# Performance work log

Measured on AMD Instinct MI355X. Metric: run time of the kernel, lower is better.

Reference implementation:

```python
import jax, jax.numpy as jnp
import numpy as np

N, IN, HID, OUT, HD = 512, 256, 256, 256, 64  # n_agents, in_dim, hid_dim, out_dim, head_dim (out_dim // n_heads)


def _mlp2(x, w1, b1, w2, b2):
    return jax.nn.relu(x @ w1.T + b1) @ w2.T + b2


def setup_inputs():
    key = jax.random.key(0)
    ks = jax.random.split(key, 32)
    p = lambda i, shape: jax.random.normal(ks[i], shape, dtype=jnp.float32) * 0.05
    V = jax.random.normal(ks[0], (N, IN), dtype=jnp.float32)
    adj = jax.random.randint(ks[1], (N, N), 0, 2, dtype=jnp.int32)
    adj = adj.at[jnp.arange(N), jnp.arange(N)].set(1)  # self-loops so no softmax row is all -inf
    prev_hidden = jax.random.normal(ks[2], (N, HID), dtype=jnp.float32)
    return {
        "V": V, "adj": adj, "prev_hidden": prev_hidden,
        "W1": p(3, (HID, IN)), "sa0": p(4, (HID,)), "sa1": p(5, (HID,)),
        "ce_w1": p(6, (HID, 2 * IN)), "ce_b1": p(7, (HID,)), "ce_w2": p(8, (HD, HID)), "ce_b2": p(9, (HD,)),
        "ca0": p(10, (HD,)), "ca1": p(11, (HD,)),
        "te_w1": p(12, (HID, IN + HID)), "te_b1": p(13, (HID,)), "te_w2": p(14, (HD, HID)), "te_b2": p(15, (HD,)),
        "ta0": p(16, (HD,)), "ta1": p(17, (HD,)),
        "pe_w1": p(18, (HID, 3 * IN)), "pe_b1": p(19, (HID,)), "pe_w2": p(20, (HD, HID)), "pe_b2": p(21, (HD,)),
        "pa0": p(22, (HD,)), "pa1": p(23, (HD,)),
        "W2": p(24, (OUT, HID + 2 * HD + 1)), "op_w": p(25, (OUT, OUT)), "op_b": p(26, (OUT,)),
        "ln_g": jnp.ones((OUT,), jnp.float32), "ln_b": jnp.zeros((OUT,), jnp.float32),
    }


def _forward(V, adj, prev_hidden, W1, sa0, sa1, ce_w1, ce_b1, ce_w2, ce_b2, ca0, ca1,
             te_w1, te_b1, te_w2, te_b2, ta0, ta1, pe_w1, pe_b1, pe_w2, pe_b2, pa0, pa1,
             W2, op_w, op_b, ln_g, ln_b):
    neg = -jnp.inf
    # --- branch 1: standard GAT attention ---
    Wh1 = V @ W1.T                                             # (N, HID)
    s1 = (Wh1 @ sa0)[:, None] + (Wh1 @ sa1)[None, :]           # (N, N)
    s1 = jnp.where(adj == 0, neg, s1)
    H1 = jax.nn.softmax(s1, axis=1) @ Wh1                      # (N, HID)
    # --- branch 2: causal, all ordered pairs i != j ---
    wA, wB = ce_w1[:, :IN], ce_w1[:, IN:]
    h = jax.nn.relu((V @ wA.T)[:, None, :] + (V @ wB.T)[None, :, :] + ce_b1)  # (N, N, HID)
    f = h @ ce_w2.T + ce_b2                                    # (N, N, HD)
    s2 = jnp.where(jnp.eye(N, dtype=bool), neg, f @ (ca0 + ca1))
    a2 = jax.nn.softmax(s2.reshape(-1)).reshape(N, N)          # softmax over all off-diagonal pairs
    H2 = jnp.broadcast_to(jnp.einsum('ij,ijd->d', a2, f), (N, HD))
    # --- branch 3: temporal; (N,1) scores broadcast against (N,N) causal mask ---
    tf = _mlp2(jnp.concatenate([V, prev_hidden], -1), te_w1, te_b1, te_w2, te_b2)  # (N, HD)
    ts = tf @ (ta0 + ta1)                                      # (N,)
    cmask = jnp.triu(jnp.ones((N, N), dtype=bool), 1)
    s3 = jnp.where(cmask, neg, jnp.broadcast_to(ts[:, None], (N, N)))
    H3 = jax.nn.softmax(s3, axis=1) @ tf                       # (N, HD) == prefix means of tf
    # --- branch 4: cooperative; first two neighbors in index order (zeros if < 2) ---
    pos = jnp.where(adj == 1, jnp.arange(N)[None, :], N)
    srt = jnp.sort(pos, axis=1)
    i0, i1 = srt[:, 0], srt[:, 1]
    valid = (i1 < N)[:, None]
    n0 = jnp.where(valid, V[jnp.clip(i0, 0, N - 1)], 0.0)
    n1 = jnp.where(valid, V[jnp.clip(i1, 0, N - 1)], 0.0)
    cf = _mlp2(jnp.concatenate([V, n0, n1], -1), pe_w1, pe_b1, pe_w2, pe_b2)  # (N, HD)
    # torch: softmax over dim of size 1 -> all ones, alpha^T @ cf == column sums -> (HD,)
    # then unsqueezed to (HD,1) and zero-padded to (N,1) since HD < N  (faithful to source bug)
    H4v = cf.sum(axis=0)
    H4 = jnp.concatenate([H4v, jnp.zeros((N - HD,), V.dtype)])[:, None]       # (N, 1)
    # --- combine ---
    Hc = jnp.concatenate([H1, H2, H3, H4], axis=-1) @ W2.T     # (N, OUT)
    out = Hc @ op_w.T + op_b
    mu = out.mean(-1, keepdims=True)
    var = ((out - mu) ** 2).mean(-1, keepdims=True)
    y = (out - mu) / jnp.sqrt(var + 1e-5) * ln_g + ln_b        # LayerNorm, eps=1e-5
    return jax.nn.elu(y)                                       # dropout is identity in eval


def reference(V, adj, prev_hidden, W1, sa0, sa1, ce_w1, ce_b1, ce_w2, ce_b2, ca0, ca1,
              te_w1, te_b1, te_w2, te_b2, ta0, ta1, pe_w1, pe_b1, pe_w2, pe_b2, pa0, pa1,
              W2, op_w, op_b, ln_g, ln_b):
    return _forward(V, adj, prev_hidden, W1, sa0, sa1, ce_w1, ce_b1, ce_w2, ce_b2, ca0, ca1,
                    te_w1, te_b1, te_w2, te_b2, ta0, ta1, pe_w1, pe_b1, pe_w2, pe_b2, pa0, pa1,
                    W2, op_w, op_b, ln_g, ln_b)
```

## Files before the change

kernel.cpp:

```cpp
#include <hip/hip_runtime.h>

typedef unsigned short u16;

constexpr int kN   = 512;
constexpr int kIN  = 256;
constexpr int kHID = 256;
constexpr int kHD  = 64;
constexpr int kOUT = 256;

__device__ __forceinline__ float us2f(u16 u){
  union { unsigned int i; float f; } c; c.i = ((unsigned int)u) << 16; return c.f;
}
__device__ __forceinline__ u16 f2us(float f){
  union { float f; unsigned int i; } c; c.f = f;
  unsigned int r = c.i + 0x7fff + ((c.i >> 16) & 1);
  return (u16)(r >> 16);
}

__device__ bool probe_is_f32(const unsigned int* __restrict__ V){
  __shared__ int cnt;
  if (threadIdx.x == 0) cnt = 0;
  __syncthreads();
  int c = 0;
  for (int k = threadIdx.x; k < 4096; k += 256){
    float x = us2f((u16)(V[k] & 0xffffu));
    if (!(fabsf(x) <= 32.0f)) c++;
  }
  atomicAdd(&cnt, c);
  __syncthreads();
  return cnt > 64;
}

struct ConvArgs { const void* src[23]; float* dst[23]; int n[23]; };

__global__ __launch_bounds__(256) void k_conv(ConvArgs a, const unsigned int* __restrict__ Vraw,
                                              const int* __restrict__ adj, int* __restrict__ flag,
                                              float* __restrict__ Xp, float* __restrict__ e1v)
{
  int b = blockIdx.x, tid = threadIdx.x;
  bool f32 = probe_is_f32(Vraw);
  if (b < 256){
    if (b == 0){
      if (tid == 0) *flag = f32 ? 1 : 0;
      e1v[tid] = 0.f; e1v[tid + 256] = 0.f;
    }
    int t = b*256 + tid;
    const int stride = 65536;
    for (int s = 0; s < 23; ++s){
      int n4 = a.n[s] >> 2;
      float4* d = (float4*)a.dst[s];
      if (f32){
        const float4* sf = (const float4*)a.src[s];
        for (int i = t; i < n4; i += stride) d[i] = sf[i];
      } else {
        const ushort4* sb = (const ushort4*)a.src[s];
        for (int i = t; i < n4; i += stride){
          ushort4 u = sb[i];
          d[i] = make_float4(us2f(u.x), us2f(u.y), us2f(u.z), us2f(u.w));
        }
      }
    }
  } else {
    __shared__ unsigned long long msk[8];
    __shared__ int sj[2];
    int i = b - 256;
    int w = tid >> 6, lane = tid & 63;
    unsigned long long m0 = __ballot(adj[(size_t)i*kN + tid] != 0);
    unsigned long long m1 = __ballot(adj[(size_t)i*kN + 256 + tid] != 0);
    if (lane == 0){ msk[w] = m0; msk[4 + w] = m1; }
    __syncthreads();
    if (tid == 0){
      int j0 = -1, j1 = -1;
      for (int c = 0; c < 8 && j1 < 0; ++c){
        unsigned long long m = msk[c];
        while (m && j1 < 0){
          int bb = __builtin_ctzll(m);
          int j = c*64 + bb;
          if (j0 < 0) j0 = j; else j1 = j;
          m &= m - 1;
        }
      }
      if (j1 < 0) j0 = -1;
      sj[0] = j0; sj[1] = j1;
    }
    __syncthreads();
    int j0 = sj[0], j1 = sj[1];
    const float* Vf = (const float*)Vraw;
    const u16*  Vb = (const u16*)Vraw;
    auto rdV = [&](int r, int k)->float{
      return f32 ? Vf[(size_t)r*kIN + k] : us2f(Vb[(size_t)r*kIN + k]);
    };
    Xp[(size_t)i*768 + tid]       = rdV(i, tid);
    Xp[(size_t)i*768 + 256 + tid] = (j0 >= 0) ? rdV(j0, tid) : 0.f;
    Xp[(size_t)i*768 + 512 + tid] = (j1 >= 0) ? rdV(j1, tid) : 0.f;
  }
}

__device__ __forceinline__ float blk_red(float v, float* tmp, bool isMax){
  int lane = threadIdx.x & 63, wv = threadIdx.x >> 6;
  #pragma unroll
  for (int o = 32; o > 0; o >>= 1){
    float t = __shfl_down(v, o, 64);
    v = isMax ? fmaxf(v, t) : (v + t);
  }
  __syncthreads();
  if (lane == 0) tmp[wv] = v;
  __syncthreads();
  float r = tmp[0];
  for (int i = 1; i < 4; ++i) r = isMax ? fmaxf(r, tmp[i]) : (r + tmp[i]);
  return r;
}

struct WSP {
  const int* adj; const int* flag; void* out;
  float *Vf,*prevf,*W1f,*sa1f,*cw1f,*cb1f,*cw2f,*cb2f,*ca0f,*ca1f;
  float *tw1f,*tb1f,*tw2f,*tb2f,*pw1f,*pb1f,*pw2f,*pb2f;
  float *W2f,*opwf,*opbf,*lngf,*lnbf;
  float *tw2t,*pw2t,*W2c,*W2midt,*w384v,*c2v;
  float *Wh1,*e1v,*minv,*invzv,*wadj,*Hc,*Am,*Bm,*uvec,*beta;
  float *s2,*maxp,*zp,*MZ,*gsum;
  float *htp0,*htp1,*hpp0,*hpp1,*hpp2,*hidden_t,*hidden_p;
  float *tfm,*cfm,*H4v,*Xp,*out2,*out3;
};

struct GSeg2 { const float* X; const float* W; float* C; int ldx, ldw, ldc, K; };
struct GArgs2 { GSeg2 s[8]; const float* sa1; float* e1; };

__global__ __launch_bounds__(256) void k_gemmA(GArgs2 ga)
{
  __shared__ __align__(16) float Xs[2][32][68];
  __shared__ __align__(16) float Ws[2][32][68];
  const GSeg2 sg = ga.s[blockIdx.y];
  const int tm = blockIdx.x & 7;
  const int tn = blockIdx.x >> 3;
  const int i0 = tm << 6;
  const int n0 = tn << 6;
  const int tid = threadIdx.x;

  const int xrow = tid >> 3;
  const int xk   = (tid & 7) << 2;
  const int rg = (tid >> 4) << 2;
  const int cg = (tid & 15) << 2;

  const float* Xb = sg.X + (size_t)i0 * sg.ldx;
  const float* Wb = sg.W + (size_t)n0 * sg.ldw;

  float4 xr0, xr1, wr0, wr1;
  auto loadT = [&](int kt){
    xr0 = *(const float4*)(Xb + (size_t)xrow * sg.ldx + kt + xk);
    xr1 = *(const float4*)(Xb + (size_t)(xrow+32) * sg.ldx + kt + xk);
    wr0 = *(const float4*)(Wb + (size_t)xrow * sg.ldw + kt + xk);
    wr1 = *(const float4*)(Wb + (size_t)(xrow+32) * sg.ldw + kt + xk);
  };
  auto writeT = [&](int bu){
    Xs[bu][xk+0][xrow] = xr0.x;  Xs[bu][xk+1][xrow] = xr0.y;
    Xs[bu][xk+2][xrow] = xr0.z;  Xs[bu][xk+3][xrow] = xr0.w;
    Xs[bu][xk+0][xrow+32] = xr1.x;  Xs[bu][xk+1][xrow+32] = xr1.y;
    Xs[bu][xk+2][xrow+32] = xr1.z;  Xs[bu][xk+3][xrow+32] = xr1.w;
    Ws[bu][xk+0][xrow]    = wr0.x; Ws[bu][xk+1][xrow]    = wr0.y;
    Ws[bu][xk+2][xrow]    = wr0.z; Ws[bu][xk+3][xrow]    = wr0.w;
    Ws[bu][xk+0][xrow+32] = wr1.x; Ws[bu][xk+1][xrow+32] = wr1.y;
    Ws[bu][xk+2][xrow+32] = wr1.z; Ws[bu][xk+3][xrow+32] = wr1.w;
  };

  loadT(0); writeT(0); __syncthreads();

  float acc[4][4] = {};
  const int nkt = sg.K >> 5;
  for (int t = 0; t < nkt; ++t){
    if (t + 1 < nkt) loadT((t + 1) << 5);
    const int bu = t & 1;
    #pragma unroll
    for (int kk = 0; kk < 32; ++kk){
      const float4 av = *(const float4*)&Xs[bu][kk][rg];
      const float4 bv = *(const float4*)&Ws[bu][kk][cg];
      acc[0][0]+=av.x*bv.x; acc[0][1]+=av.x*bv.y; acc[0][2]+=av.x*bv.z; acc[0][3]+=av.x*bv.w;
      acc[1][0]+=av.y*bv.x; acc[1][1]+=av.y*bv.y; acc[1][2]+=av.y*bv.z; acc[1][3]+=av.y*bv.w;
      acc[2][0]+=av.z*bv.x; acc[2][1]+=av.z*bv.y; acc[2][2]+=av.z*bv.z; acc[2][3]+=av.z*bv.w;
      acc[3][0]+=av.w*bv.x; acc[3][1]+=av.w*bv.y; acc[3][2]+=av.w*bv.z; acc[3][3]+=av.w*bv.w;
    }
    if (t + 1 < nkt) writeT((t + 1) & 1);
    __syncthreads();
  }

  #pragma unroll
  for (int ri = 0; ri < 4; ++ri)
    *(float4*)(sg.C + (size_t)(i0 + rg + ri) * sg.ldc + (n0 + cg)) =
      make_float4(acc[ri][0], acc[ri][1], acc[ri][2], acc[ri][3]);

  if (blockIdx.y == 0){
    int cb = n0 + cg;
    float s0 = ga.sa1[cb], s1 = ga.sa1[cb+1], s2v = ga.sa1[cb+2], s3 = ga.sa1[cb+3];
    #pragma unroll
    for (int ri = 0; ri < 4; ++ri){
      float v = acc[ri][0]*s0 + acc[ri][1]*s1 + acc[ri][2]*s2v + acc[ri][3]*s3;
      v += __shfl_xor(v, 1, 16);
      v += __shfl_xor(v, 2, 16);
      v += __shfl_xor(v, 4, 16);
      v += __shfl_xor(v, 8, 16);
      if ((tid & 15) == 0) atomicAdd(&ga.e1[i0 + rg + ri], v);
    }
  }
}

struct GS32 { const float* X; const float* W; float* C; int ldx, ldw, ldc, K;
              const float* c2; const float* w384; const float* h4; int bkn; };

__device__ __forceinline__ void gemm32_body(const GS32 sg, int tm, int tn, int tid,
                                            float* Xs, float* Ws)
{
  const int i0 = tm << 5, n0 = tn << 5;
  const int xrow = tid >> 3;
  const int xk = (tid & 7) << 2;
  const int rg = (tid >> 4) << 1;
  const int cg = (tid & 15) << 1;
  const float* Xb = sg.X + (size_t)i0 * sg.ldx;
  const float* Wb = sg.bkn ? (sg.W + n0) : (sg.W + (size_t)n0 * sg.ldw);
  float h4r = 0.f;
  if (sg.h4){ int i = i0 + xrow; h4r = (i < 64) ? sg.h4[i] : 0.f; }
  float4 xr, wr;
  auto loadT = [&](int kt){
    xr = *(const float4*)(Xb + (size_t)xrow * sg.ldx + kt + xk);
    if (sg.bkn) wr = *(const float4*)(Wb + (size_t)(kt + xrow) * sg.ldw + xk);
    else        wr = *(const float4*)(Wb + (size_t)xrow * sg.ldw + kt + xk);
    if (sg.c2){
      float4 c = *(const float4*)(sg.c2 + kt + xk);
      float4 w3 = *(const float4*)(sg.w384 + kt + xk);
      xr.x += c.x + h4r*w3.x; xr.y += c.y + h4r*w3.y;
      xr.z += c.z + h4r*w3.z; xr.w += c.w + h4r*w3.w;
    }
  };
  auto writeT = [&](int bu){
    float* xs = Xs + bu*1152;
    xs[(xk+0)*36 + xrow] = xr.x; xs[(xk+1)*36 + xrow] = xr.y;
    xs[(xk+2)*36 + xrow] = xr.z; xs[(xk+3)*36 + xrow] = xr.w;
    float* wsp = Ws + bu*1152;
    if (sg.bkn){
      wsp[xrow*36 + xk+0] = wr.x; wsp[xrow*36 + xk+1] = wr.y;
      wsp[xrow*36 + xk+2] = wr.z; wsp[xrow*36 + xk+3] = wr.w;
    } else {
      wsp[(xk+0)*36 + xrow] = wr.x; wsp[(xk+1)*36 + xrow] = wr.y;
      wsp[(xk+2)*36 + xrow] = wr.z; wsp[(xk+3)*36 + xrow] = wr.w;
    }
  };
  loadT(0); writeT(0); __syncthreads();
  float a00=0,a01=0,a10=0,a11=0;
  const int nkt = sg.K >> 5;
  for (int t = 0; t < nkt; ++t){
    if (t+1 < nkt) loadT((t+1) << 5);
    const float* xs = Xs + (t&1)*1152;
    const float* wsp = Ws + (t&1)*1152;
    #pragma unroll
    for (int kk = 0; kk < 32; ++kk){
      float2 av = *(const float2*)&xs[kk*36 + rg];
      float2 bv = *(const float2*)&wsp[kk*36 + cg];
      a00 += av.x*bv.x; a01 += av.x*bv.y;
      a10 += av.y*bv.x; a11 += av.y*bv.y;
    }
    if (t+1 < nkt) writeT((t+1)&1);
    __syncthreads();
  }
  float* cp = sg.C + (size_t)(i0+rg)*sg.ldc + n0 + cg;
  *(float2*)cp = make_float2(a00, a01);
  *(float2*)(cp + sg.ldc) = make_float2(a10, a11);
}

__global__ __launch_bounds__(256) void k_stage2(WSP w)
{
  __shared__ float st[64*65];
  int b = blockIdx.x, tid = threadIdx.x;
  if (b < 128){
    int f = b*256 + tid;
    int c4 = f & 63;
    {
      float4 a = ((const float4*)w.htp0)[f], bb = ((const float4*)w.htp1)[f];
      float4 bi = ((const float4*)w.tb1f)[c4];
      ((float4*)w.hidden_t)[f] = make_float4(
        fmaxf(a.x+bb.x+bi.x,0.f), fmaxf(a.y+bb.y+bi.y,0.f),
        fmaxf(a.z+bb.z+bi.z,0.f), fmaxf(a.w+bb.w+bi.w,0.f));
    }
    {
      float4 a = ((const float4*)w.hpp0)[f], bb = ((const float4*)w.hpp1)[f];
      float4 c = ((const float4*)w.hpp2)[f];
      float4 bi = ((const float4*)w.pb1f)[c4];
      ((float4*)w.hidden_p)[f] = make_float4(
        fmaxf(a.x+bb.x+c.x+bi.x,0.f), fmaxf(a.y+bb.y+c.y+bi.y,0.f),
        fmaxf(a.z+bb.z+c.z+bi.z,0.f), fmaxf(a.w+bb.w+c.w+bi.w,0.f));
    }
  } else if (b < 640){
    float* red = st;
    int i = b - 128;
    int m0 = w.adj[(size_t)i*kN + tid];
    int m1 = w.adj[(size_t)i*kN + tid + 256];
    float ea = w.e1v[tid], eb = w.e1v[tid+256];
    float v0 = m0 ? ea : -1e30f;
    float v1 = m1 ? eb : -1e30f;
    float m = blk_red(fmaxf(v0, v1), red, true);
    float z = blk_red((m0 ? expf(ea-m) : 0.f) + (m1 ? expf(eb-m) : 0.f), red, false);
    if (tid == 0){ w.minv[i] = m; w.invzv[i] = 1.0f / z; }
  } else if (b == 640){
    if (tid < 64){ st[tid] = w.ca0f[tid] + w.ca1f[tid]; w.H4v[tid] = 0.f; }
    __syncthreads();
    float a = 0.f;
    for (int d = 0; d < kHD; ++d) a += w.cw2f[(size_t)d*kHID + tid] * st[d];
    w.uvec[tid] = a;
    if (tid == 0){
      float bsum = 0.f;
      for (int d = 0; d < kHD; ++d) bsum += w.cb2f[d] * st[d];
      *w.beta = bsum;
    }
  } else if (b < 643){
    const float* src = (b == 641) ? w.tw2f : w.pw2f;
    float* dst = (b == 641) ? w.tw2t : w.pw2t;
    for (int ch = 0; ch < 4; ++ch){
      __syncthreads();
      #pragma unroll
      for (int e = 0; e < 16; ++e){
        int lin = e*256 + tid;
        int r = lin >> 6, c = lin & 63;
        st[r*65 + c] = src[(size_t)r*256 + ch*64 + c];
      }
      __syncthreads();
      #pragma unroll
      for (int e = 0; e < 16; ++e){
        int lin = e*256 + tid;
        int kc = lin >> 6, dd = lin & 63;
        dst[(size_t)(ch*64 + kc)*64 + dd] = st[dd*65 + kc];
      }
    }
  } else if (b < 707){
    int o0 = (b - 643) * 4;
    for (int r = 0; r < 4; ++r){
      int o = o0 + r;
      const float* src = w.W2f + (size_t)o * 385;
      float* dst = w.W2c + (size_t)o * 320;
      for (int c = tid; c < 320; c += 256)
        dst[c] = src[(c < 256) ? c : c + 64];
    }
  } else if (b < 723){
    int d0 = (b - 707) * 4;
    #pragma unroll
    for (int dd = 0; dd < 4; ++dd)
      w.W2midt[(size_t)(d0+dd)*256 + tid] = w.W2f[(size_t)tid*385 + 256 + d0 + dd];
  } else {
    w.w384v[tid] = w.W2f[(size_t)tid*385 + 384];
  }
}

__global__ __launch_bounds__(256) void k_stage3(WSP w)
{
  __shared__ __align__(16) float smem3[4*256 + 256];
  int b = blockIdx.x, tid = threadIdx.x;
  if (b < 64){
    int m = b >> 5, grp = b & 31;
    const float* X  = m ? w.hidden_p : w.hidden_t;
    const float* Wt = m ? w.pw2t : w.tw2t;
    const float* bi = m ? w.pb2f : w.tb2f;
    float* C = m ? w.cfm : w.tfm;
    int i0 = grp*16 + (tid >> 6)*4;
    int d = tid & 63;
    const float* x0 = X + (size_t)i0*256;
    const float* x1 = x0 + 256;
    const float* x2 = x0 + 512;
    const float* x3 = x0 + 768;
    float a0=0.f, a1=0.f, a2=0.f, a3=0.f;
    for (int k = 0; k < 256; k += 4){
      float w0 = Wt[(size_t)(k+0)*64 + d];
      float w1 = Wt[(size_t)(k+1)*64 + d];
      float w2 = Wt[(size_t)(k+2)*64 + d];
      float w3 = Wt[(size_t)(k+3)*64 + d];
      float4 f0 = *(const float4*)(x0 + k);
      float4 f1 = *(const float4*)(x1 + k);
      float4 f2 = *(const float4*)(x2 + k);
      float4 f3 = *(const float4*)(x3 + k);
      a0 += f0.x*w0 + f0.y*w1 + f0.z*w2 + f0.w*w3;
      a1 += f1.x*w0 + f1.y*w1 + f1.z*w2 + f1.w*w3;
      a2 += f2.x*w0 + f2.y*w1 + f2.z*w2 + f2.w*w3;
      a3 += f3.x*w0 + f3.y*w1 + f3.z*w2 + f3.w*w3;
    }
    float bd = bi[d];
    C[(size_t)(i0+0)*64 + d] = a0 + bd;
    C[(size_t)(i0+1)*64 + d] = a1 + bd;
    C[(size_t)(i0+2)*64 + d] = a2 + bd;
    C[(size_t)(i0+3)*64 + d] = a3 + bd;
  } else if (b < 576){
    int i = b - 64;
    float mi = w.minv[i], zi = w.invzv[i];
    w.wadj[(size_t)i*kN + tid] =
      w.adj[(size_t)i*kN + tid] ? expf(w.e1v[tid] - mi) * zi : 0.f;
    w.wadj[(size_t)i*kN + tid + 256] =
      w.adj[(size_t)i*kN + tid + 256] ? expf(w.e1v[tid+256] - mi) * zi : 0.f;
  } else {
    float* aib = smem3;
    float* uu  = smem3 + 1024;
    int q = b - 576;
    int i0 = (q & 127) * 4, j0 = (q >> 7) * 64;
    int wv = tid >> 6, lane = tid & 63;
    uu[tid] = w.uvec[tid];
    float b1v = w.cb1f[tid];
    #pragma unroll
    for (int r = 0; r < 4; ++r) aib[r*256 + tid] = w.Am[(size_t)(i0+r)*kHID + tid] + b1v;
    __syncthreads();
    int i = i0 + wv, j = j0 + lane;
    const float4* bp = (const float4*)(w.Bm + (size_t)j*kHID);
    float acc = *w.beta;
    #pragma unroll 8
    for (int k4 = 0; k4 < kHID/4; ++k4){
      float4 bv = bp[k4];
      float4 a4 = *(const float4*)&aib[wv*256 + k4*4];
      float4 u4 = *(const float4*)&uu[k4*4];
      acc += fmaxf(a4.x+bv.x,0.f)*u4.x + fmaxf(a4.y+bv.y,0.f)*u4.y
           + fmaxf(a4.z+bv.z,0.f)*u4.z + fmaxf(a4.w+bv.w,0.f)*u4.w;
    }
    if (j == i) acc = -1e30f;
    w.s2[(size_t)i*kN + j] = acc;
    float m = acc;
    #pragma unroll
    for (int o = 32; o > 0; o >>= 1) m = fmaxf(m, __shfl_down(m, o, 64));
    m = __shfl(m, 0, 64);
    float e = expf(acc - m);
    #pragma unroll
    for (int o = 32; o > 0; o >>= 1) e += __shfl_down(e, o, 64);
    if (lane == 0){
      int pb = q*4 + wv;
      w.maxp[pb] = m; w.zp[pb] = e;
    }
  }
}

__global__ __launch_bounds__(256) void k_stage4(WSP w)
{
  __shared__ __align__(16) char smem[18432];
  int b = blockIdx.x, tid = threadIdx.x;
  if (b < 128){
    GS32 sg{w.wadj, w.Wh1, w.Hc, 512, 256, 320, 512, nullptr, nullptr, nullptr, 1};
    gemm32_body(sg, b & 15, b >> 4, tid, (float*)smem, (float*)(smem + 9216));
  } else if (b < 192){
    int d = b - 128;
    int lane = tid & 63, wv = tid >> 6;
    float v0 = w.tfm[(size_t)(2*tid)*kHD + d];
    float v1 = w.tfm[(size_t)(2*tid+1)*kHD + d];
    float s = v0 + v1;
    float x = s;
    #pragma unroll
    for (int off = 1; off < 64; off <<= 1){
      float y = __shfl_up(x, off, 64);
      if (lane >= off) x += y;
    }
    float* wsum = (float*)smem;
    if (lane == 63) wsum[wv] = x;
    __syncthreads();
    float base = 0.f;
    for (int k = 0; k < wv; ++k) base += wsum[k];
    float excl = base + x - s;
    w.Hc[(size_t)(2*tid)*320 + 256 + d]   = (excl + v0) / (float)(2*tid + 1);
    w.Hc[(size_t)(2*tid+1)*320 + 256 + d] = (excl + s)  / (float)(2*tid + 2);
  } else if (b < 200){
    float* sm = (float*)smem;
    int d = tid & 63, sub = tid >> 6;
    int r0 = (b-192)*64 + sub*16;
    float s = 0.f;
    #pragma unroll
    for (int e = 0; e < 16; ++e) s += w.cfm[(size_t)(r0+e)*kHD + d];
    sm[sub*64 + d] = s;
    __syncthreads();
    if (tid < 64)
      atomicAdd(&w.H4v[tid], sm[tid] + sm[64+tid] + sm[128+tid] + sm[192+tid]);
  } else {
    float* red = (float*)smem;
    float m = -1e30f;
    #pragma unroll
    for (int r = 0; r < 16; ++r) m = fmaxf(m, w.maxp[tid + 256*r]);
    m = blk_red(m, red, true);
    float z = 0.f;
    #pragma unroll
    for (int r = 0; r < 16; ++r) z += w.zp[tid + 256*r] * expf(w.maxp[tid + 256*r] - m);
    z = blk_red(z, red, false);
    if (tid == 0){ w.MZ[0] = m; w.MZ[1] = z; }
    w.gsum[tid] = 0.f;
  }
}

__global__ __launch_bounds__(256) void k_stage5(WSP w)
{
  __shared__ __align__(16) char smem[18432];
  int b = blockIdx.x, tid = threadIdx.x;
  if (b < 1024){
    float* wt = (float*)smem;
    int i0 = (b & 31) * 16, j0 = (b >> 5) * 16;
    float M = w.MZ[0], invZ = 1.0f / w.MZ[1];
    {
      int r = tid >> 4, c = tid & 15;
      wt[r*16 + c] = expf(w.s2[(size_t)(i0+r)*kN + (j0+c)] - M) * invZ;
    }
    float b1v = w.cb1f[tid];
    float aib[16];
    #pragma unroll
    for (int r = 0; r < 16; ++r) aib[r] = w.Am[(size_t)(i0+r)*kHID + tid] + b1v;
    __syncthreads();
    float acc = 0.f;
    for (int j = 0; j < 16; ++j){
      float bj = w.Bm[(size_t)(j0+j)*kHID + tid];
      #pragma unroll
      for (int r = 0; r < 16; ++r)
        acc += wt[r*16 + j] * fmaxf(aib[r] + bj, 0.f);
    }
    atomicAdd(&w.gsum[tid], acc);
  } else {
    int q = b - 1024;
    GS32 sg{w.Hc, w.W2c, w.out2, 320, 320, 256, 320, nullptr, nullptr, nullptr, 0};
    gemm32_body(sg, q & 15, q >> 4, tid, (float*)smem, (float*)(smem + 9216));
  }
}

__global__ void k_h2c(WSP w)
{
  __shared__ float gs[kHID];
  __shared__ float part[kHD][4];
  __shared__ float h2s[kHD];
  int tid = threadIdx.x;
  gs[tid] = w.gsum[tid];
  __syncthreads();
  int dd = tid >> 2, q = tid & 3;
  float a = 0.f;
  for (int kk = 0; kk < 64; ++kk){
    int k = q*64 + kk;
    a += gs[k] * w.cw2f[(size_t)dd*kHID + k];
  }
  part[dd][q] = a;
  __syncthreads();
  if (tid < kHD)
    h2s[tid] = w.cb2f[tid] + part[tid][0] + part[tid][1] + part[tid][2] + part[tid][3];
  __syncthreads();
  float c = 0.f;
  for (int d = 0; d < kHD; ++d) c += h2s[d] * w.W2midt[(size_t)d*256 + tid];
  w.c2v[tid] = c;
}

__global__ __launch_bounds__(256) void k_out3g(WSP w)
{
  __shared__ __align__(16) char smem[18432];
  GS32 sg{w.out2, w.opwf, w.out3, 256, 256, 256, 256, w.c2v, w.w384v, w.H4v, 0};
  gemm32_body(sg, blockIdx.x & 15, blockIdx.x >> 4, threadIdx.x, (float*)smem, (float*)(smem + 9216));
}

__global__ __launch_bounds__(256) void k_final(WSP w)
{
  int b = blockIdx.x, tid = threadIdx.x;
  int row = b*4 + (tid >> 6), lane = tid & 63;
  float4 v = *(const float4*)(w.out3 + (size_t)row*kOUT + lane*4);
  float4 pb = *(const float4*)(w.opbf + lane*4);
  v.x += pb.x; v.y += pb.y; v.z += pb.z; v.w += pb.w;
  float s = v.x + v.y + v.z + v.w;
  #pragma unroll
  for (int o = 32; o > 0; o >>= 1) s += __shfl_xor(s, o, 64);
  float mu = s * (1.0f/kOUT);
  float dx = v.x-mu, dy = v.y-mu, dz = v.z-mu, dw = v.w-mu;
  float ss = dx*dx + dy*dy + dz*dz + dw*dw;
  #pragma unroll
  for (int o = 32; o > 0; o >>= 1) ss += __shfl_xor(ss, o, 64);
  float rs = rsqrtf(ss * (1.0f/kOUT) + 1e-5f);
  float4 g = *(const float4*)(w.lngf + lane*4);
  float4 be = *(const float4*)(w.lnbf + lane*4);
  float y0 = dx*rs*g.x + be.x, y1 = dy*rs*g.y + be.y;
  float y2 = dz*rs*g.z + be.z, y3 = dw*rs*g.w + be.w;
  y0 = (y0 > 0.f) ? y0 : expm1f(y0);
  y1 = (y1 > 0.f) ? y1 : expm1f(y1);
  y2 = (y2 > 0.f) ? y2 : expm1f(y2);
  y3 = (y3 > 0.f) ? y3 : expm1f(y3);
  if (*w.flag){
    *(float4*)((float*)w.out + (size_t)row*kOUT + lane*4) = make_float4(y0,y1,y2,y3);
  } else {
    ushort4 u; u.x = f2us(y0); u.y = f2us(y1); u.z = f2us(y2); u.w = f2us(y3);
    ((ushort4*)w.out)[(size_t)row*64 + lane] = u;
  }
}

extern "C" void kernel_launch(void* const* d_in, const int* in_sizes, int n_in,
                              void* d_out, int out_size, void* d_ws, size_t ws_size,
                              hipStream_t stream)
{
  const void* V     = d_in[0];
  const int*  adj   = (const int*)d_in[1];
  const void* prev  = d_in[2];
  const void* W1    = d_in[3];
  const void* sa1   = d_in[5];
  const void* ce_w1 = d_in[6];
  const void* ce_b1 = d_in[7];
  const void* ce_w2 = d_in[8];
  const void* ce_b2 = d_in[9];
  const void* ca0   = d_in[10];
  const void* ca1   = d_in[11];
  const void* te_w1 = d_in[12];
  const void* te_b1 = d_in[13];
  const void* te_w2 = d_in[14];
  const void* te_b2 = d_in[15];
  const void* pe_w1 = d_in[18];
  const void* pe_b1 = d_in[19];
  const void* pe_w2 = d_in[20];
  const void* pe_b2 = d_in[21];
  const void* W2    = d_in[24];
  const void* op_w  = d_in[25];
  const void* op_b  = d_in[26];
  const void* ln_g  = d_in[27];
  const void* ln_b  = d_in[28];

  float* ws  = (float*)d_ws;
  int*  flag = (int*)ws;
  float* p   = ws + 16;
  float* Vf   = p; p += 131072;
  float* prevf= p; p += 131072;
  float* W1f  = p; p += 65536;
  float* sa1f = p; p += 256;
  float* cw1f = p; p += 131072;
  float* cb1f = p; p += 256;
  float* cw2f = p; p += 16384;
  float* cb2f = p; p += 64;
  float* ca0f = p; p += 64;
  float* ca1f = p; p += 64;
  float* tw1f = p; p += 131072;
  float* tb1f = p; p += 256;
  float* tw2f = p; p += 16384;
  float* tb2f = p; p += 64;
  float* pw1f = p; p += 196608;
  float* pb1f = p; p += 256;
  float* pw2f = p; p += 16384;
  float* pb2f = p; p += 64;
  float* W2f  = p; p += 98560;
  float* opwf = p; p += 65536;
  float* opbf = p; p += 256;
  float* lngf = p; p += 256;
  float* lnbf = p; p += 256;
  float* tw2t = p; p += 16384;
  float* pw2t = p; p += 16384;
  float* W2c  = p; p += 81920;
  float* W2midt = p; p += 16384;
  float* w384v  = p; p += 256;
  float* c2v    = p; p += 256;
  float* Wh1      = p; p += 131072;
  float* e1v      = p; p += 512;
  float* minv     = p; p += 512;
  float* invzv    = p; p += 512;
  float* wadj     = p; p += 262144;
  float* Hc       = p; p += 163840;
  float* Am       = p; p += 131072;
  float* Bm       = p; p += 131072;
  float* uvec     = p; p += 256;
  float* beta     = p; p += 16;
  float* s2       = p; p += 262144;
  float* maxp     = p; p += 4096;
  float* zpart    = p; p += 4096;
  float* MZ       = p; p += 16;
  float* gsum     = p; p += 256;
  float* htp0     = p; p += 131072;
  float* htp1     = p; p += 131072;
  float* hpp0     = p; p += 131072;
  float* hpp1     = p; p += 131072;
  float* hpp2     = p; p += 131072;
  float* hidden_t = p; p += 131072;
  float* hidden_p = p; p += 131072;
  float* tfm      = p; p += 32768;
  float* cfm      = p; p += 32768;
  float* H4v      = p; p += 64;
  float* Xp       = p; p += 393216;
  float* out2     = p; p += 131072;
  float* out3     = p; p += 131072;

  WSP w;
  w.adj = adj; w.flag = flag; w.out = d_out;
  w.Vf=Vf; w.prevf=prevf; w.W1f=W1f; w.sa1f=sa1f; w.cw1f=cw1f; w.cb1f=cb1f;
  w.cw2f=cw2f; w.cb2f=cb2f; w.ca0f=ca0f; w.ca1f=ca1f;
  w.tw1f=tw1f; w.tb1f=tb1f; w.tw2f=tw2f; w.tb2f=tb2f;
  w.pw1f=pw1f; w.pb1f=pb1f; w.pw2f=pw2f; w.pb2f=pb2f;
  w.W2f=W2f; w.opwf=opwf; w.opbf=opbf; w.lngf=lngf; w.lnbf=lnbf;
  w.tw2t=tw2t; w.pw2t=pw2t; w.W2c=W2c; w.W2midt=W2midt; w.w384v=w384v; w.c2v=c2v;
  w.Wh1=Wh1; w.e1v=e1v; w.minv=minv; w.invzv=invzv; w.wadj=wadj; w.Hc=Hc;
  w.Am=Am; w.Bm=Bm; w.uvec=uvec; w.beta=beta;
  w.s2=s2; w.maxp=maxp; w.zp=zpart; w.MZ=MZ; w.gsum=gsum;
  w.htp0=htp0; w.htp1=htp1; w.hpp0=hpp0; w.hpp1=hpp1; w.hpp2=hpp2;
  w.hidden_t=hidden_t; w.hidden_p=hidden_p;
  w.tfm=tfm; w.cfm=cfm; w.H4v=H4v; w.Xp=Xp; w.out2=out2; w.out3=out3;

  {
    ConvArgs ca;
    const void* srcs[23] = {V, prev, W1, sa1, ce_w1, ce_b1, ce_w2, ce_b2, ca0, ca1,
                            te_w1, te_b1, te_w2, te_b2, pe_w1, pe_b1, pe_w2, pe_b2,
                            W2, op_w, op_b, ln_g, ln_b};
    float* dsts[23] = {Vf, prevf, W1f, sa1f, cw1f, cb1f, cw2f, cb2f, ca0f, ca1f,
                       tw1f, tb1f, tw2f, tb2f, pw1f, pb1f, pw2f, pb2f,
                       W2f, opwf, opbf, lngf, lnbf};
    int ns[23] = {131072, 131072, 65536, 256, 131072, 256, 16384, 64, 64, 64,
                  131072, 256, 16384, 64, 196608, 256, 16384, 64,
                  98560, 65536, 256, 256, 256};
    for (int s = 0; s < 23; ++s){ ca.src[s] = srcs[s]; ca.dst[s] = dsts[s]; ca.n[s] = ns[s]; }
    k_conv<<<768, 256, 0, stream>>>(ca, (const unsigned int*)V, adj, flag, Xp, e1v);
  }

  {
    GArgs2 g{};
    g.s[0] = {Vf,       W1f,        Wh1,  256, 256, 256, 256};
    g.s[1] = {Vf,       cw1f,       Am,   256, 512, 256, 256};
    g.s[2] = {Vf,       cw1f + 256, Bm,   256, 512, 256, 256};
    g.s[3] = {Vf,       tw1f,       htp0, 256, 512, 256, 256};
    g.s[4] = {prevf,    tw1f + 256, htp1, 256, 512, 256, 256};
    g.s[5] = {Xp,       pw1f,       hpp0, 768, 768, 256, 256};
    g.s[6] = {Xp + 256, pw1f + 256, hpp1, 768, 768, 256, 256};
    g.s[7] = {Xp + 512, pw1f + 512, hpp2, 768, 768, 256, 256};
    g.sa1 = sa1f; g.e1 = e1v;
    k_gemmA<<<dim3(32, 8), 256, 0, stream>>>(g);
  }

  k_stage2<<<724, 256, 0, stream>>>(w);

  k_stage3<<<1600, 256, 0, stream>>>(w);

  k_stage4<<<201, 256, 0, stream>>>(w);

  k_stage5<<<1152, 256, 0, stream>>>(w);

  k_h2c<<<1, 256, 0, stream>>>(w);

  k_out3g<<<128, 256, 0, stream>>>(w);

  k_final<<<128, 256, 0, stream>>>(w);
}
```

Baseline: 243.5 us.

## Fold output projection into W2 weights and compute attention weights during softmax stats

Precomputes op_w·W2 (the combined weight, the middle-column product and the last-column vector) in stage2 so the final Hc GEMM writes out3 directly. This removes the separate out2→op_w GEMM kernel and the single-block h2c kernel; the rank-1 and low-rank corrections move into k_final. The softmax-stat blocks now write the normalized adjacency weights directly, which drops 512 blocks from stage3 and the minv/invz buffers. Two kernel launches and one full N×OUT GEMM pass are removed. In exchange, stage2 does extra small GEMMs and each k_final block redundantly recomputes h2 and the c2 vector.

After: 243.0 us. About the same (-0.2%).

```diff
diff --git a/kernel.cpp b/kernel.cpp
--- a/kernel.cpp
+++ b/kernel.cpp
@@ -116,11 +116,11 @@
   float *Vf,*prevf,*W1f,*sa1f,*cw1f,*cb1f,*cw2f,*cb2f,*ca0f,*ca1f;
   float *tw1f,*tb1f,*tw2f,*tb2f,*pw1f,*pb1f,*pw2f,*pb2f;
   float *W2f,*opwf,*opbf,*lngf,*lnbf;
-  float *tw2t,*pw2t,*W2c,*W2midt,*w384v,*c2v;
-  float *Wh1,*e1v,*minv,*invzv,*wadj,*Hc,*Am,*Bm,*uvec,*beta;
+  float *tw2t,*pw2t,*Wcomb,*OM,*ow4;
+  float *Wh1,*e1v,*wadj,*Hc,*Am,*Bm,*uvec,*beta;
   float *s2,*maxp,*zp,*MZ,*gsum;
   float *htp0,*htp1,*hpp0,*hpp1,*hpp2,*hidden_t,*hidden_p;
-  float *tfm,*cfm,*H4v,*Xp,*out2,*out3;
+  float *tfm,*cfm,*H4v,*Xp,*out3;
 };
 
 struct GSeg2 { const float* X; const float* W; float* C; int ldx, ldw, ldc, K; };
@@ -203,8 +203,7 @@
   }
 }
 
-struct GS32 { const float* X; const float* W; float* C; int ldx, ldw, ldc, K;
-              const float* c2; const float* w384; const float* h4; int bkn; };
+struct GS32 { const float* X; const float* W; float* C; int ldx, ldw, ldc, K; int bkn; };
 
 __device__ __forceinline__ void gemm32_body(const GS32 sg, int tm, int tn, int tid,
                                             float* Xs, float* Ws)
@@ -216,19 +215,11 @@
   const int cg = (tid & 15) << 1;
   const float* Xb = sg.X + (size_t)i0 * sg.ldx;
   const float* Wb = sg.bkn ? (sg.W + n0) : (sg.W + (size_t)n0 * sg.ldw);
-  float h4r = 0.f;
-  if (sg.h4){ int i = i0 + xrow; h4r = (i < 64) ? sg.h4[i] : 0.f; }
   float4 xr, wr;
   auto loadT = [&](int kt){
     xr = *(const float4*)(Xb + (size_t)xrow * sg.ldx + kt + xk);
     if (sg.bkn) wr = *(const float4*)(Wb + (size_t)(kt + xrow) * sg.ldw + xk);
     else        wr = *(const float4*)(Wb + (size_t)xrow * sg.ldw + kt + xk);
-    if (sg.c2){
-      float4 c = *(const float4*)(sg.c2 + kt + xk);
-      float4 w3 = *(const float4*)(sg.w384 + kt + xk);
-      xr.x += c.x + h4r*w3.x; xr.y += c.y + h4r*w3.y;
-      xr.z += c.z + h4r*w3.z; xr.w += c.w + h4r*w3.w;
-    }
   };
   auto writeT = [&](int bu){
     float* xs = Xs + bu*1152;
@@ -267,7 +258,8 @@
 
 __global__ __launch_bounds__(256) void k_stage2(WSP w)
 {
-  __shared__ float st[64*65];
+  __shared__ __align__(16) char smem[18432];
+  float* st = (float*)smem;
   int b = blockIdx.x, tid = threadIdx.x;
   if (b < 128){
     int f = b*256 + tid;
@@ -288,16 +280,17 @@
         fmaxf(a.z+bb.z+c.z+bi.z,0.f), fmaxf(a.w+bb.w+c.w+bi.w,0.f));
     }
   } else if (b < 640){
-    float* red = st;
     int i = b - 128;
     int m0 = w.adj[(size_t)i*kN + tid];
     int m1 = w.adj[(size_t)i*kN + tid + 256];
     float ea = w.e1v[tid], eb = w.e1v[tid+256];
     float v0 = m0 ? ea : -1e30f;
     float v1 = m1 ? eb : -1e30f;
-    float m = blk_red(fmaxf(v0, v1), red, true);
-    float z = blk_red((m0 ? expf(ea-m) : 0.f) + (m1 ? expf(eb-m) : 0.f), red, false);
-    if (tid == 0){ w.minv[i] = m; w.invzv[i] = 1.0f / z; }
+    float m = blk_red(fmaxf(v0, v1), st, true);
+    float z = blk_red((m0 ? expf(ea-m) : 0.f) + (m1 ? expf(eb-m) : 0.f), st, false);
+    float iz = 1.0f / z;
+    w.wadj[(size_t)i*kN + tid]       = m0 ? expf(ea - m) * iz : 0.f;
+    w.wadj[(size_t)i*kN + tid + 256] = m1 ? expf(eb - m) * iz : 0.f;
   } else if (b == 640){
     if (tid < 64){ st[tid] = w.ca0f[tid] + w.ca1f[tid]; w.H4v[tid] = 0.f; }
     __syncthreads();
@@ -328,22 +321,26 @@
         dst[(size_t)(ch*64 + kc)*64 + dd] = st[dd*65 + kc];
       }
     }
-  } else if (b < 707){
-    int o0 = (b - 643) * 4;
-    for (int r = 0; r < 4; ++r){
-      int o = o0 + r;
-      const float* src = w.W2f + (size_t)o * 385;
-      float* dst = w.W2c + (size_t)o * 320;
-      for (int c = tid; c < 320; c += 256)
-        dst[c] = src[(c < 256) ? c : c + 64];
-    }
   } else if (b < 723){
-    int d0 = (b - 707) * 4;
-    #pragma unroll
-    for (int dd = 0; dd < 4; ++dd)
-      w.W2midt[(size_t)(d0+dd)*256 + tid] = w.W2f[(size_t)tid*385 + 256 + d0 + dd];
+    int q = b - 643;
+    int tm = q & 7, tn = q >> 3;
+    const float* Wsrc = w.W2f + ((tn < 8) ? 0 : 64);
+    GS32 sg{w.opwf, Wsrc, w.Wcomb, 256, 385, 320, 256, 1};
+    gemm32_body(sg, tm, tn, tid, (float*)smem, (float*)(smem + 9216));
+  } else if (b < 739){
+    int q = b - 723;
+    GS32 sg{w.opwf, w.W2f + 256, w.OM, 256, 385, 64, 256, 1};
+    gemm32_body(sg, q & 7, q >> 3, tid, (float*)smem, (float*)(smem + 9216));
   } else {
-    w.w384v[tid] = w.W2f[(size_t)tid*385 + 384];
+    st[tid] = w.W2f[(size_t)tid*385 + 384];
+    __syncthreads();
+    float a = 0.f;
+    const float* orow = w.opwf + (size_t)tid*256;
+    for (int m = 0; m < 256; m += 4){
+      float4 o4 = *(const float4*)(orow + m);
+      a += o4.x*st[m] + o4.y*st[m+1] + o4.z*st[m+2] + o4.w*st[m+3];
+    }
+    w.ow4[tid] = a;
   }
 }
 
@@ -383,17 +380,10 @@
     C[(size_t)(i0+1)*64 + d] = a1 + bd;
     C[(size_t)(i0+2)*64 + d] = a2 + bd;
     C[(size_t)(i0+3)*64 + d] = a3 + bd;
-  } else if (b < 576){
-    int i = b - 64;
-    float mi = w.minv[i], zi = w.invzv[i];
-    w.wadj[(size_t)i*kN + tid] =
-      w.adj[(size_t)i*kN + tid] ? expf(w.e1v[tid] - mi) * zi : 0.f;
-    w.wadj[(size_t)i*kN + tid + 256] =
-      w.adj[(size_t)i*kN + tid + 256] ? expf(w.e1v[tid+256] - mi) * zi : 0.f;
   } else {
     float* aib = smem3;
     float* uu  = smem3 + 1024;
-    int q = b - 576;
+    int q = b - 64;
     int i0 = (q & 127) * 4, j0 = (q >> 7) * 64;
     int wv = tid >> 6, lane = tid & 63;
     uu[tid] = w.uvec[tid];
@@ -433,7 +423,7 @@
   __shared__ __align__(16) char smem[18432];
   int b = blockIdx.x, tid = threadIdx.x;
   if (b < 128){
-    GS32 sg{w.wadj, w.Wh1, w.Hc, 512, 256, 320, 512, nullptr, nullptr, nullptr, 1};
+    GS32 sg{w.wadj, w.Wh1, w.Hc, 512, 256, 320, 512, 1};
     gemm32_body(sg, b & 15, b >> 4, tid, (float*)smem, (float*)(smem + 9216));
   } else if (b < 192){
     int d = b - 128;
@@ -508,49 +498,53 @@
     atomicAdd(&w.gsum[tid], acc);
   } else {
     int q = b - 1024;
-    GS32 sg{w.Hc, w.W2c, w.out2, 320, 320, 256, 320, nullptr, nullptr, nullptr, 0};
+    GS32 sg{w.Hc, w.Wcomb, w.out3, 320, 320, 256, 320, 0};
     gemm32_body(sg, q & 15, q >> 4, tid, (float*)smem, (float*)(smem + 9216));
   }
 }
 
-__global__ void k_h2c(WSP w)
+__global__ __launch_bounds__(256) void k_final(WSP w)
 {
   __shared__ float gs[kHID];
   __shared__ float part[kHD][4];
   __shared__ float h2s[kHD];
-  int tid = threadIdx.x;
+  __shared__ float cc2s[kOUT];
+  int b = blockIdx.x, tid = threadIdx.x;
   gs[tid] = w.gsum[tid];
   __syncthreads();
-  int dd = tid >> 2, q = tid & 3;
-  float a = 0.f;
-  for (int kk = 0; kk < 64; ++kk){
-    int k = q*64 + kk;
-    a += gs[k] * w.cw2f[(size_t)dd*kHID + k];
-  }
-  part[dd][q] = a;
+  {
+    int dd = tid >> 2, q = tid & 3;
+    float a = 0.f;
+    for (int kk = 0; kk < 64; ++kk){
+      int k = q*64 + kk;
+      a += gs[k] * w.cw2f[(size_t)dd*kHID + k];
+    }
+    part[dd][q] = a;
+  }
   __syncthreads();
   if (tid < kHD)
     h2s[tid] = w.cb2f[tid] + part[tid][0] + part[tid][1] + part[tid][2] + part[tid][3];
   __syncthreads();
-  float c = 0.f;
-  for (int d = 0; d < kHD; ++d) c += h2s[d] * w.W2midt[(size_t)d*256 + tid];
-  w.c2v[tid] = c;
-}
-
-__global__ __launch_bounds__(256) void k_out3g(WSP w)
-{
-  __shared__ __align__(16) char smem[18432];
-  GS32 sg{w.out2, w.opwf, w.out3, 256, 256, 256, 256, w.c2v, w.w384v, w.H4v, 0};
-  gemm32_body(sg, blockIdx.x & 15, blockIdx.x >> 4, threadIdx.x, (float*)smem, (float*)(smem + 9216));
-}
-
-__global__ __launch_bounds__(256) void k_final(WSP w)
-{
-  int b = blockIdx.x, tid = threadIdx.x;
+  {
+    float a = 0.f;
+    const float* om = w.OM + (size_t)tid*64;
+    for (int d = 0; d < kHD; d += 4){
+      float4 o4 = *(const float4*)(om + d);
+      a += o4.x*h2s[d] + o4.y*h2s[d+1] + o4.z*h2s[d+2] + o4.w*h2s[d+3];
+    }
+    cc2s[tid] = a;
+  }
+  __syncthreads();
   int row = b*4 + (tid >> 6), lane = tid & 63;
-  float4 v = *(const float4*)(w.out3 + (size_t)row*kOUT + lane*4);
+  float h4r = (row < kHD) ? w.H4v[row] : 0.f;
+  float4 v  = *(const float4*)(w.out3 + (size_t)row*kOUT + lane*4);
+  float4 c2 = *(const float4*)(&cc2s[lane*4]);
+  float4 o4 = *(const float4*)(w.ow4 + lane*4);
   float4 pb = *(const float4*)(w.opbf + lane*4);
-  v.x += pb.x; v.y += pb.y; v.z += pb.z; v.w += pb.w;
+  v.x += c2.x + h4r*o4.x + pb.x;
+  v.y += c2.y + h4r*o4.y + pb.y;
+  v.z += c2.z + h4r*o4.z + pb.z;
+  v.w += c2.w + h4r*o4.w + pb.w;
   float s = v.x + v.y + v.z + v.w;
   #pragma unroll
   for (int o = 32; o > 0; o >>= 1) s += __shfl_xor(s, o, 64);
@@ -560,7 +554,7 @@
   #pragma unroll
   for (int o = 32; o > 0; o >>= 1) ss += __shfl_xor(ss, o, 64);
   float rs = rsqrtf(ss * (1.0f/kOUT) + 1e-5f);
-  float4 g = *(const float4*)(w.lngf + lane*4);
+  float4 g  = *(const float4*)(w.lngf + lane*4);
   float4 be = *(const float4*)(w.lnbf + lane*4);
   float y0 = dx*rs*g.x + be.x, y1 = dy*rs*g.y + be.y;
   float y2 = dz*rs*g.z + be.z, y3 = dw*rs*g.w + be.w;
@@ -633,14 +627,11 @@
   float* lnbf = p; p += 256;
   float* tw2t = p; p += 16384;
   float* pw2t = p; p += 16384;
-  float* W2c  = p; p += 81920;
-  float* W2midt = p; p += 16384;
-  float* w384v  = p; p += 256;
-  float* c2v    = p; p += 256;
+  float* Wcomb= p; p += 81920;
+  float* OM   = p; p += 16384;
+  float* ow4  = p; p += 256;
   float* Wh1      = p; p += 131072;
   float* e1v      = p; p += 512;
-  float* minv     = p; p += 512;
-  float* invzv    = p; p += 512;
   float* wadj     = p; p += 262144;
   float* Hc       = p; p += 163840;
   float* Am       = p; p += 131072;
@@ -663,7 +654,6 @@
   float* cfm      = p; p += 32768;
   float* H4v      = p; p += 64;
   float* Xp       = p; p += 393216;
-  float* out2     = p; p += 131072;
   float* out3     = p; p += 131072;
 
   WSP w;
@@ -673,13 +663,13 @@
   w.tw1f=tw1f; w.tb1f=tb1f; w.tw2f=tw2f; w.tb2f=tb2f;
   w.pw1f=pw1f; w.pb1f=pb1f; w.pw2f=pw2f; w.pb2f=pb2f;
   w.W2f=W2f; w.opwf=opwf; w.opbf=opbf; w.lngf=lngf; w.lnbf=lnbf;
-  w.tw2t=tw2t; w.pw2t=pw2t; w.W2c=W2c; w.W2midt=W2midt; w.w384v=w384v; w.c2v=c2v;
-  w.Wh1=Wh1; w.e1v=e1v; w.minv=minv; w.invzv=invzv; w.wadj=wadj; w.Hc=Hc;
+  w.tw2t=tw2t; w.pw2t=pw2t; w.Wcomb=Wcomb; w.OM=OM; w.ow4=ow4;
+  w.Wh1=Wh1; w.e1v=e1v; w.wadj=wadj; w.Hc=Hc;
   w.Am=Am; w.Bm=Bm; w.uvec=uvec; w.beta=beta;
   w.s2=s2; w.maxp=maxp; w.zp=zpart; w.MZ=MZ; w.gsum=gsum;
   w.htp0=htp0; w.htp1=htp1; w.hpp0=hpp0; w.hpp1=hpp1; w.hpp2=hpp2;
   w.hidden_t=hidden_t; w.hidden_p=hidden_p;
-  w.tfm=tfm; w.cfm=cfm; w.H4v=H4v; w.Xp=Xp; w.out2=out2; w.out3=out3;
+  w.tfm=tfm; w.cfm=cfm; w.H4v=H4v; w.Xp=Xp; w.out3=out3;
 
   {
     ConvArgs ca;
@@ -710,17 +700,13 @@
     k_gemmA<<<dim3(32, 8), 256, 0, stream>>>(g);
   }
 
-  k_stage2<<<724, 256, 0, stream>>>(w);
-
-  k_stage3<<<1600, 256, 0, stream>>>(w);
+  k_stage2<<<740, 256, 0, stream>>>(w);
+
+  k_stage3<<<1088, 256, 0, stream>>>(w);
 
   k_stage4<<<201, 256, 0, stream>>>(w);
 
   k_stage5<<<1152, 256, 0, stream>>>(w);
 
-  k_h2c<<<1, 256, 0, stream>>>(w);
-
-  k_out3g<<<128, 256, 0, stream>>>(w);
-
   k_final<<<128, 256, 0, stream>>>(w);
 }
```
